# Performance work log

Measured on AMD Instinct MI355X. Metric: run time of the kernel, lower is better.

The kernel has to match this reference:

```python
import jax, jax.numpy as jnp
import numpy as np

N, D, F_IN, F_MID, F_OUT = 200000, 3, 128, 512, 128


def setup_inputs() -> dict:
    key = jax.random.key(0)
    ks = jax.random.split(key, 6)
    s = lambda fan_in: 1.0 / np.sqrt(fan_in)
    return {
        "x": jax.random.normal(ks[0], (N, D, F_IN), dtype=jnp.float32),
        "W_prop": jax.random.normal(ks[1], (F_IN, F_OUT), dtype=jnp.float32) * s(F_IN),
        "W1": jax.random.normal(ks[2], (F_IN, F_MID), dtype=jnp.float32) * s(F_IN),
        "b1": jax.random.normal(ks[3], (F_MID,), dtype=jnp.float32) * s(F_IN),
        "W2": jax.random.normal(ks[4], (F_MID, F_OUT), dtype=jnp.float32) * s(F_MID),
        "b2": jax.random.normal(ks[5], (F_OUT,), dtype=jnp.float32) * s(F_MID),
    }


def reference(x, W_prop, W1, b1, W2, b2):
    # linear_weight (Proportional): bias-free linear on the feature axis,
    # applied to the rank-1 equivariant tensor -> stays equivariant.
    linear_x = jnp.einsum("ndf,fg->ndg", x, W_prop)  # [N, D, F_OUT]
    # contraction(x): invariant inner product over spatial components.
    c = jnp.einsum("ndf,ndf->nf", x, x)  # [N, F_IN]
    # norm_function = identity; MLP chain: Linear->tanh->Linear->identity
    h = jnp.tanh(c @ W1 + b1)  # [N, F_MID]
    h = h @ W2 + b2            # [N, F_OUT]
    # tensor_product(rank-1, rank-0): broadcast multiply over spatial dim.
    return linear_x * h[:, None, :]  # [N, D, F_OUT]
```

## Files before the change

kernel.cpp:

```cpp
#include <hip/hip_runtime.h>
#include <hip/hip_bf16.h>

#define NROWS   200000
#define TILE    16
#define NBLOCKS (NROWS / TILE)

typedef __attribute__((ext_vector_type(4))) float f32x4;
typedef __attribute__((ext_vector_type(8))) short bf16x8;

__device__ __forceinline__ unsigned pk2(float lo, float hi) {
  float2 f{lo, hi};
  __hip_bfloat162 h = __float22bfloat162_rn(f);
  unsigned u;
  __builtin_memcpy(&u, &h, 4);
  return u;
}
__device__ __forceinline__ unsigned short f2bf(float f) {
  unsigned b = __float_as_uint(f);
  b += 0x7fffu + ((b >> 16) & 1u);
  return (unsigned short)(b >> 16);
}
__device__ __forceinline__ float bflo(unsigned pk) { return __uint_as_float(pk << 16); }
__device__ __forceinline__ float bfhi(unsigned pk) { return __uint_as_float(pk & 0xffff0000u); }
__device__ __forceinline__ f32x4 mfma16(bf16x8 a, bf16x8 b, f32x4 c) {
  return __builtin_amdgcn_mfma_f32_16x16x32_bf16(a, b, c, 0, 0, 0);
}
__device__ __forceinline__ float fast_tanh(float x) {
  float e = __expf(2.0f * x);
  return 1.0f - __fdividef(2.0f, e + 1.0f);
}
__device__ __forceinline__ int SW(int b) { return b ^ (((b >> 8) & 7) << 4); }

__global__ void prep_weights(const float* __restrict__ Wp,
                             const float* __restrict__ W1,
                             const float* __restrict__ W2,
                             unsigned short* __restrict__ wpf,
                             unsigned short* __restrict__ w1f,
                             unsigned short* __restrict__ w2f) {
  int t = blockIdx.x * 256 + threadIdx.x;
  int q = t >> 6, l = t & 63;
  const float* W; unsigned short* dst; int NT, Nout, qb;
  if (q < 32)       { W = Wp; dst = wpf; NT = 8;  Nout = 128; qb = q; }
  else if (q < 160) { W = W1; dst = w1f; NT = 32; Nout = 512; qb = q - 32; }
  else              { W = W2; dst = w2f; NT = 8;  Nout = 128; qb = q - 160; }
  int kt = qb / NT, nt = qb % NT;
  int row0 = kt * 32 + 8 * (l >> 4);
  int col  = (nt >> 1) * 32 + 2 * (l & 15) + (nt & 1);
  unsigned short v[8];
#pragma unroll
  for (int i = 0; i < 8; ++i) v[i] = f2bf(W[(row0 + i) * Nout + col]);
  uint4 pack;
  pack.x = (unsigned)v[0] | ((unsigned)v[1] << 16);
  pack.y = (unsigned)v[2] | ((unsigned)v[3] << 16);
  pack.z = (unsigned)v[4] | ((unsigned)v[5] << 16);
  pack.w = (unsigned)v[6] | ((unsigned)v[7] << 16);
  *(uint4*)(dst + (size_t)(qb * 64 + l) * 8) = pack;
}

__global__ __launch_bounds__(256, 4) void fused_kernel(
    const float* __restrict__ x,
    const float* __restrict__ b1,
    const float* __restrict__ b2,
    const unsigned short* __restrict__ wpf,
    const unsigned short* __restrict__ w1f,
    const unsigned short* __restrict__ w2f,
    float* __restrict__ out) {
  __shared__ __align__(16) char smem[16384];
  const int t = threadIdx.x;
  const int l = t & 63;
  const int w = t >> 6;
  const int lr = l & 15;
  const int lq = l >> 4;
  const long n0 = (long)blockIdx.x * TILE;

  {
    const int r = t >> 4;
    const int f0 = (t & 15) * 8;
    const float* xp = x + (n0 + r) * 384 + f0;
    float4 a0 = *(const float4*)(xp);
    float4 a1 = *(const float4*)(xp + 4);
    float4 b0 = *(const float4*)(xp + 128);
    float4 b1_ = *(const float4*)(xp + 132);
    float4 c0 = *(const float4*)(xp + 256);
    float4 c1 = *(const float4*)(xp + 260);
    uint4 sa = { pk2(a0.x, a0.y), pk2(a0.z, a0.w), pk2(a1.x, a1.y), pk2(a1.z, a1.w) };
    uint4 sb = { pk2(b0.x, b0.y), pk2(b0.z, b0.w), pk2(b1_.x, b1_.y), pk2(b1_.z, b1_.w) };
    uint4 sc = { pk2(c0.x, c0.y), pk2(c0.z, c0.w), pk2(c1.x, c1.y), pk2(c1.z, c1.w) };
    uint4 cv = { pk2(a0.x*a0.x + b0.x*b0.x + c0.x*c0.x,
                     a0.y*a0.y + b0.y*b0.y + c0.y*c0.y),
                 pk2(a0.z*a0.z + b0.z*b0.z + c0.z*c0.z,
                     a0.w*a0.w + b0.w*b0.w + c0.w*c0.w),
                 pk2(a1.x*a1.x + b1_.x*b1_.x + c1.x*c1.x,
                     a1.y*a1.y + b1_.y*b1_.y + c1.y*c1.y),
                 pk2(a1.z*a1.z + b1_.z*b1_.z + c1.z*c1.z,
                     a1.w*a1.w + b1_.w*b1_.w + c1.w*c1.w) };
    *(uint4*)(smem + SW((3 * r + 0) * 256 + f0 * 2)) = sa;
    *(uint4*)(smem + SW((3 * r + 1) * 256 + f0 * 2)) = sb;
    *(uint4*)(smem + SW((3 * r + 2) * 256 + f0 * 2)) = sc;
    *(uint4*)(smem + SW(12288 + r * 256 + f0 * 2))   = cv;
  }
  __syncthreads();

  unsigned lx[3][4];
  {
    f32x4 acc1[3][2] = {};
#pragma unroll
    for (int kt = 0; kt < 4; ++kt) {
      bf16x8 a[3];
#pragma unroll
      for (int m = 0; m < 3; ++m)
        a[m] = *(const bf16x8*)(smem + SW((m * 16 + lr) * 256 + kt * 64 + lq * 16));
#pragma unroll
      for (int jj = 0; jj < 2; ++jj) {
        bf16x8 b = *(const bf16x8*)(wpf + (size_t)((kt * 8 + 2 * w + jj) * 64 + l) * 8);
#pragma unroll
        for (int m = 0; m < 3; ++m) acc1[m][jj] = mfma16(a[m], b, acc1[m][jj]);
      }
    }
#pragma unroll
    for (int m = 0; m < 3; ++m)
#pragma unroll
      for (int reg = 0; reg < 4; ++reg)
        lx[m][reg] = pk2(acc1[m][0][reg], acc1[m][1][reg]);
  }

  f32x4 acc2[2];
  auto do_gemm2 = [&](int ch) {
    { f32x4 z = {}; acc2[0] = z; acc2[1] = z; }
#pragma unroll
    for (int kt = 0; kt < 4; ++kt) {
      bf16x8 a2 = *(const bf16x8*)(smem + SW(12288 + lr * 256 + kt * 64 + lq * 16));
#pragma unroll
      for (int jj = 0; jj < 2; ++jj) {
        bf16x8 b = *(const bf16x8*)(w1f + (size_t)((kt * 32 + ch * 8 + 2 * w + jj) * 64 + l) * 8);
        acc2[jj] = mfma16(a2, b, acc2[jj]);
      }
    }
  };

  f32x4 acc3[2] = {};
  do_gemm2(0);
  __syncthreads();

#pragma unroll
  for (int ch = 0; ch < 4; ++ch) {
    {
      const int bufb = (ch & 1) * 4096;
      float2 b1v = *(const float2*)(b1 + ch * 128 + w * 32 + 2 * lr);
#pragma unroll
      for (int reg = 0; reg < 4; ++reg) {
        int row = 4 * lq + reg;
        unsigned pk = pk2(fast_tanh(acc2[0][reg] + b1v.x),
                          fast_tanh(acc2[1][reg] + b1v.y));
        *(unsigned*)(smem + SW(bufb + row * 256 + w * 64 + 4 * lr)) = pk;
      }
    }
    if (ch < 3) do_gemm2(ch + 1);
    __syncthreads();
    {
      const int bufb = (ch & 1) * 4096;
#pragma unroll
      for (int kt = 0; kt < 4; ++kt) {
        bf16x8 a3 = *(const bf16x8*)(smem + SW(bufb + lr * 256 + kt * 64 + lq * 16));
#pragma unroll
        for (int jj = 0; jj < 2; ++jj) {
          bf16x8 b = *(const bf16x8*)(w2f + (size_t)(((ch * 4 + kt) * 8 + 2 * w + jj) * 64 + l) * 8);
          acc3[jj] = mfma16(a3, b, acc3[jj]);
        }
      }
    }
  }

  {
    float2 b2v = *(const float2*)(b2 + w * 32 + 2 * lr);
#pragma unroll
    for (int reg = 0; reg < 4; ++reg) {
      int row = 4 * lq + reg;
      *(unsigned*)(smem + SW(8192 + row * 256 + w * 64 + 4 * lr)) =
          pk2(acc3[0][reg] + b2v.x, acc3[1][reg] + b2v.y);
    }
  }
  __syncthreads();

#pragma unroll
  for (int m = 0; m < 3; ++m)
#pragma unroll
    for (int reg = 0; reg < 4; ++reg) {
      int rp = m * 16 + 4 * lq + reg;
      int n = rp / 3;
      unsigned hp = *(const unsigned*)(smem + SW(8192 + n * 256 + w * 64 + 4 * lr));
      unsigned pk = lx[m][reg];
      float2 o = { bflo(pk) * bflo(hp), bfhi(pk) * bfhi(hp) };
      *(float2*)(out + n0 * 384 + (long)rp * 128 + w * 32 + 2 * lr) = o;
    }
}

extern "C" void kernel_launch(void* const* d_in, const int* in_sizes, int n_in,
                              void* d_out, int out_size, void* d_ws, size_t ws_size,
                              hipStream_t stream) {
  const float* x  = (const float*)d_in[0];
  const float* Wp = (const float*)d_in[1];
  const float* W1 = (const float*)d_in[2];
  const float* b1 = (const float*)d_in[3];
  const float* W2 = (const float*)d_in[4];
  const float* b2 = (const float*)d_in[5];
  float* out = (float*)d_out;

  if (ws_size < 294912) return;
  unsigned short* w1f = (unsigned short*)d_ws;
  unsigned short* w2f = (unsigned short*)((char*)d_ws + 131072);
  unsigned short* wpf = (unsigned short*)((char*)d_ws + 262144);

  prep_weights<<<72, 256, 0, stream>>>(Wp, W1, W2, wpf, w1f, w2f);
  fused_kernel<<<NBLOCKS, 256, 0, stream>>>(x, b1, b2, wpf, w1f, w2f, out);
}
```

Before: 226.8 us.

## Enlarge row tile to 64 with 512-thread blocks to amortize weight loads

Increases rows per block from 16 to 64 and threads from 256 to 512. Each weight fragment loaded from global memory now feeds four M-tiles instead of one, so W1/W2 traffic per row drops. The W1/W2 layout changes from interleaved column pairs to contiguous 16-column tiles. The software-pipelined GEMM2 prefetch is removed, and LDS use grows to 64KB, which may limit occupancy to fewer blocks per CU than before.

```diff
diff --git a/kernel.cpp b/kernel.cpp
--- a/kernel.cpp
+++ b/kernel.cpp
@@ -2,7 +2,7 @@
 #include <hip/hip_bf16.h>
 
 #define NROWS   200000
-#define TILE    16
+#define TILE    64
 #define NBLOCKS (NROWS / TILE)
 
 typedef __attribute__((ext_vector_type(4))) float f32x4;
@@ -14,6 +14,9 @@
   unsigned u;
   __builtin_memcpy(&u, &h, 4);
   return u;
+}
+__device__ __forceinline__ unsigned short bf1(float v) {
+  return (unsigned short)pk2(v, v);
 }
 __device__ __forceinline__ unsigned short f2bf(float f) {
   unsigned b = __float_as_uint(f);
@@ -39,13 +42,14 @@
                              unsigned short* __restrict__ w2f) {
   int t = blockIdx.x * 256 + threadIdx.x;
   int q = t >> 6, l = t & 63;
-  const float* W; unsigned short* dst; int NT, Nout, qb;
-  if (q < 32)       { W = Wp; dst = wpf; NT = 8;  Nout = 128; qb = q; }
-  else if (q < 160) { W = W1; dst = w1f; NT = 32; Nout = 512; qb = q - 32; }
-  else              { W = W2; dst = w2f; NT = 8;  Nout = 128; qb = q - 160; }
+  const float* W; unsigned short* dst; int NT, Nout, qb; bool inter;
+  if (q < 32)       { W = Wp; dst = wpf; NT = 8;  Nout = 128; qb = q;       inter = true;  }
+  else if (q < 160) { W = W1; dst = w1f; NT = 32; Nout = 512; qb = q - 32;  inter = false; }
+  else              { W = W2; dst = w2f; NT = 8;  Nout = 128; qb = q - 160; inter = false; }
   int kt = qb / NT, nt = qb % NT;
   int row0 = kt * 32 + 8 * (l >> 4);
-  int col  = (nt >> 1) * 32 + 2 * (l & 15) + (nt & 1);
+  int col  = inter ? (nt >> 1) * 32 + 2 * (l & 15) + (nt & 1)
+                   : nt * 16 + (l & 15);
   unsigned short v[8];
 #pragma unroll
   for (int i = 0; i < 8; ++i) v[i] = f2bf(W[(row0 + i) * Nout + col]);
@@ -57,7 +61,7 @@
   *(uint4*)(dst + (size_t)(qb * 64 + l) * 8) = pack;
 }
 
-__global__ __launch_bounds__(256, 4) void fused_kernel(
+__global__ __launch_bounds__(512, 4) void fused_kernel(
     const float* __restrict__ x,
     const float* __restrict__ b1,
     const float* __restrict__ b2,
@@ -65,54 +69,63 @@
     const unsigned short* __restrict__ w1f,
     const unsigned short* __restrict__ w2f,
     float* __restrict__ out) {
-  __shared__ __align__(16) char smem[16384];
+  __shared__ __align__(16) char smem[65536];
   const int t = threadIdx.x;
   const int l = t & 63;
   const int w = t >> 6;
   const int lr = l & 15;
   const int lq = l >> 4;
+  const int p = w & 3;
+  const int h = w >> 2;
   const long n0 = (long)blockIdx.x * TILE;
 
   {
-    const int r = t >> 4;
-    const int f0 = (t & 15) * 8;
+    const int r = t >> 3;
+    const int f0 = (t & 7) * 16;
     const float* xp = x + (n0 + r) * 384 + f0;
-    float4 a0 = *(const float4*)(xp);
-    float4 a1 = *(const float4*)(xp + 4);
-    float4 b0 = *(const float4*)(xp + 128);
-    float4 b1_ = *(const float4*)(xp + 132);
-    float4 c0 = *(const float4*)(xp + 256);
-    float4 c1 = *(const float4*)(xp + 260);
-    uint4 sa = { pk2(a0.x, a0.y), pk2(a0.z, a0.w), pk2(a1.x, a1.y), pk2(a1.z, a1.w) };
-    uint4 sb = { pk2(b0.x, b0.y), pk2(b0.z, b0.w), pk2(b1_.x, b1_.y), pk2(b1_.z, b1_.w) };
-    uint4 sc = { pk2(c0.x, c0.y), pk2(c0.z, c0.w), pk2(c1.x, c1.y), pk2(c1.z, c1.w) };
-    uint4 cv = { pk2(a0.x*a0.x + b0.x*b0.x + c0.x*c0.x,
-                     a0.y*a0.y + b0.y*b0.y + c0.y*c0.y),
-                 pk2(a0.z*a0.z + b0.z*b0.z + c0.z*c0.z,
-                     a0.w*a0.w + b0.w*b0.w + c0.w*c0.w),
-                 pk2(a1.x*a1.x + b1_.x*b1_.x + c1.x*c1.x,
-                     a1.y*a1.y + b1_.y*b1_.y + c1.y*c1.y),
-                 pk2(a1.z*a1.z + b1_.z*b1_.z + c1.z*c1.z,
-                     a1.w*a1.w + b1_.w*b1_.w + c1.w*c1.w) };
-    *(uint4*)(smem + SW((3 * r + 0) * 256 + f0 * 2)) = sa;
-    *(uint4*)(smem + SW((3 * r + 1) * 256 + f0 * 2)) = sb;
-    *(uint4*)(smem + SW((3 * r + 2) * 256 + f0 * 2)) = sc;
-    *(uint4*)(smem + SW(12288 + r * 256 + f0 * 2))   = cv;
+#pragma unroll
+    for (int hh = 0; hh < 2; ++hh) {
+      float4 a0 = *(const float4*)(xp + hh * 8);
+      float4 a1 = *(const float4*)(xp + hh * 8 + 4);
+      float4 b0 = *(const float4*)(xp + 128 + hh * 8);
+      float4 b1_ = *(const float4*)(xp + 132 + hh * 8);
+      float4 c0 = *(const float4*)(xp + 256 + hh * 8);
+      float4 c1 = *(const float4*)(xp + 260 + hh * 8);
+      uint4 sa = { pk2(a0.x, a0.y), pk2(a0.z, a0.w), pk2(a1.x, a1.y), pk2(a1.z, a1.w) };
+      uint4 sb = { pk2(b0.x, b0.y), pk2(b0.z, b0.w), pk2(b1_.x, b1_.y), pk2(b1_.z, b1_.w) };
+      uint4 sc = { pk2(c0.x, c0.y), pk2(c0.z, c0.w), pk2(c1.x, c1.y), pk2(c1.z, c1.w) };
+      uint4 cv = { pk2(a0.x*a0.x + b0.x*b0.x + c0.x*c0.x,
+                       a0.y*a0.y + b0.y*b0.y + c0.y*c0.y),
+                   pk2(a0.z*a0.z + b0.z*b0.z + c0.z*c0.z,
+                       a0.w*a0.w + b0.w*b0.w + c0.w*c0.w),
+                   pk2(a1.x*a1.x + b1_.x*b1_.x + c1.x*c1.x,
+                       a1.y*a1.y + b1_.y*b1_.y + c1.y*c1.y),
+                   pk2(a1.z*a1.z + b1_.z*b1_.z + c1.z*c1.z,
+                       a1.w*a1.w + b1_.w*b1_.w + c1.w*c1.w) };
+      const int fb = (f0 + hh * 8) * 2;
+      *(uint4*)(smem + SW((3 * r + 0) * 256 + fb)) = sa;
+      *(uint4*)(smem + SW((3 * r + 1) * 256 + fb)) = sb;
+      *(uint4*)(smem + SW((3 * r + 2) * 256 + fb)) = sc;
+      *(uint4*)(smem + SW(49152 + r * 256 + fb))   = cv;
+    }
   }
   __syncthreads();
 
-  unsigned lx[3][4];
-  {
+  unsigned lx[6][4];
+#pragma unroll
+  for (int s = 0; s < 2; ++s) {
     f32x4 acc1[3][2] = {};
 #pragma unroll
     for (int kt = 0; kt < 4; ++kt) {
       bf16x8 a[3];
 #pragma unroll
-      for (int m = 0; m < 3; ++m)
-        a[m] = *(const bf16x8*)(smem + SW((m * 16 + lr) * 256 + kt * 64 + lq * 16));
+      for (int m = 0; m < 3; ++m) {
+        int row = h * 96 + (s * 3 + m) * 16 + lr;
+        a[m] = *(const bf16x8*)(smem + SW(row * 256 + kt * 64 + lq * 16));
+      }
 #pragma unroll
       for (int jj = 0; jj < 2; ++jj) {
-        bf16x8 b = *(const bf16x8*)(wpf + (size_t)((kt * 8 + 2 * w + jj) * 64 + l) * 8);
+        bf16x8 b = *(const bf16x8*)(wpf + (size_t)((kt * 8 + 2 * p + jj) * 64 + l) * 8);
 #pragma unroll
         for (int m = 0; m < 3; ++m) acc1[m][jj] = mfma16(a[m], b, acc1[m][jj]);
       }
@@ -121,77 +134,70 @@
     for (int m = 0; m < 3; ++m)
 #pragma unroll
       for (int reg = 0; reg < 4; ++reg)
-        lx[m][reg] = pk2(acc1[m][0][reg], acc1[m][1][reg]);
-  }
-
-  f32x4 acc2[2];
-  auto do_gemm2 = [&](int ch) {
-    { f32x4 z = {}; acc2[0] = z; acc2[1] = z; }
+        lx[s * 3 + m][reg] = pk2(acc1[m][0][reg], acc1[m][1][reg]);
+  }
+
+  f32x4 acc3[4] = {};
+#pragma unroll
+  for (int ch = 0; ch < 4; ++ch) {
+    f32x4 acc2[4] = {};
 #pragma unroll
     for (int kt = 0; kt < 4; ++kt) {
-      bf16x8 a2 = *(const bf16x8*)(smem + SW(12288 + lr * 256 + kt * 64 + lq * 16));
-#pragma unroll
-      for (int jj = 0; jj < 2; ++jj) {
-        bf16x8 b = *(const bf16x8*)(w1f + (size_t)((kt * 32 + ch * 8 + 2 * w + jj) * 64 + l) * 8);
-        acc2[jj] = mfma16(a2, b, acc2[jj]);
-      }
-    }
-  };
-
-  f32x4 acc3[2] = {};
-  do_gemm2(0);
+      bf16x8 b = *(const bf16x8*)(w1f + (size_t)((kt * 32 + ch * 8 + w) * 64 + l) * 8);
+#pragma unroll
+      for (int m = 0; m < 4; ++m) {
+        bf16x8 a2 = *(const bf16x8*)(smem + SW(49152 + (m * 16 + lr) * 256 + kt * 64 + lq * 16));
+        acc2[m] = mfma16(a2, b, acc2[m]);
+      }
+    }
+    if (ch == 0) __syncthreads();
+    const int bufb = (ch & 1) * 16384;
+    {
+      float b1v = b1[ch * 128 + w * 16 + lr];
+#pragma unroll
+      for (int m = 0; m < 4; ++m)
+#pragma unroll
+        for (int reg = 0; reg < 4; ++reg) {
+          int row = m * 16 + 4 * lq + reg;
+          *(unsigned short*)(smem + SW(bufb + row * 256 + (w * 16 + lr) * 2)) =
+              bf1(fast_tanh(acc2[m][reg] + b1v));
+        }
+    }
+    __syncthreads();
+#pragma unroll
+    for (int kt = 0; kt < 4; ++kt) {
+      bf16x8 b = *(const bf16x8*)(w2f + (size_t)(((ch * 4 + kt) * 8 + w) * 64 + l) * 8);
+#pragma unroll
+      for (int m = 0; m < 4; ++m) {
+        bf16x8 a3 = *(const bf16x8*)(smem + SW(bufb + (m * 16 + lr) * 256 + kt * 64 + lq * 16));
+        acc3[m] = mfma16(a3, b, acc3[m]);
+      }
+    }
+  }
+
+  {
+    float b2v = b2[w * 16 + lr];
+#pragma unroll
+    for (int m = 0; m < 4; ++m)
+#pragma unroll
+      for (int reg = 0; reg < 4; ++reg) {
+        int row = m * 16 + 4 * lq + reg;
+        *(unsigned short*)(smem + SW(32768 + row * 256 + (w * 16 + lr) * 2)) =
+            bf1(acc3[m][reg] + b2v);
+      }
+  }
   __syncthreads();
 
 #pragma unroll
-  for (int ch = 0; ch < 4; ++ch) {
-    {
-      const int bufb = (ch & 1) * 4096;
-      float2 b1v = *(const float2*)(b1 + ch * 128 + w * 32 + 2 * lr);
-#pragma unroll
-      for (int reg = 0; reg < 4; ++reg) {
-        int row = 4 * lq + reg;
-        unsigned pk = pk2(fast_tanh(acc2[0][reg] + b1v.x),
-                          fast_tanh(acc2[1][reg] + b1v.y));
-        *(unsigned*)(smem + SW(bufb + row * 256 + w * 64 + 4 * lr)) = pk;
-      }
-    }
-    if (ch < 3) do_gemm2(ch + 1);
-    __syncthreads();
-    {
-      const int bufb = (ch & 1) * 4096;
-#pragma unroll
-      for (int kt = 0; kt < 4; ++kt) {
-        bf16x8 a3 = *(const bf16x8*)(smem + SW(bufb + lr * 256 + kt * 64 + lq * 16));
-#pragma unroll
-        for (int jj = 0; jj < 2; ++jj) {
-          bf16x8 b = *(const bf16x8*)(w2f + (size_t)(((ch * 4 + kt) * 8 + 2 * w + jj) * 64 + l) * 8);
-          acc3[jj] = mfma16(a3, b, acc3[jj]);
-        }
-      }
-    }
-  }
-
-  {
-    float2 b2v = *(const float2*)(b2 + w * 32 + 2 * lr);
+  for (int m = 0; m < 6; ++m)
 #pragma unroll
     for (int reg = 0; reg < 4; ++reg) {
-      int row = 4 * lq + reg;
-      *(unsigned*)(smem + SW(8192 + row * 256 + w * 64 + 4 * lr)) =
-          pk2(acc3[0][reg] + b2v.x, acc3[1][reg] + b2v.y);
-    }
-  }
-  __syncthreads();
-
-#pragma unroll
-  for (int m = 0; m < 3; ++m)
-#pragma unroll
-    for (int reg = 0; reg < 4; ++reg) {
-      int rp = m * 16 + 4 * lq + reg;
+      int rp = h * 96 + m * 16 + 4 * lq + reg;
       int n = rp / 3;
-      unsigned hp = *(const unsigned*)(smem + SW(8192 + n * 256 + w * 64 + 4 * lr));
+      unsigned hp = *(const unsigned*)(smem + SW(32768 + n * 256 + (p * 32 + 2 * lr) * 2));
       unsigned pk = lx[m][reg];
       float2 o = { bflo(pk) * bflo(hp), bfhi(pk) * bfhi(hp) };
-      *(float2*)(out + n0 * 384 + (long)rp * 128 + w * 32 + 2 * lr) = o;
+      *(float2*)(out + n0 * 384 + (long)rp * 128 + p * 32 + 2 * lr) = o;
     }
 }
 
@@ -212,5 +218,5 @@
   unsigned short* wpf = (unsigned short*)((char*)d_ws + 262144);
 
   prep_weights<<<72, 256, 0, stream>>>(Wp, W1, W2, wpf, w1f, w2f);
-  fused_kernel<<<NBLOCKS, 256, 0, stream>>>(x, b1, b2, wpf, w1f, w2f, out);
-}
+  fused_kernel<<<NBLOCKS, 512, 0, stream>>>(x, b1, b2, wpf, w1f, w2f, out);
+}
```

Result: slower. 325.0 us (+43.3%).
